# Kernel optimization log

Hardware: AMD Instinct MI355X
Metric: run time of the kernel (lower is better)

Reference implementation:

```python
import jax, jax.numpy as jnp
import numpy as np

SEQ, BATCH, D_MODEL = 1536, 2, 1024
N_HEAD, D_HEAD, N_ROLL = 16, 64, 3
SCALE = 1.0 / float(np.sqrt(D_HEAD))
EPS_DENOM = 1e-5
EPS_LN = 1e-5


def _dpfp(x, n_roll=N_ROLL):
    # relu feature map: cat(relu(x), relu(-x)), then roll-multiply expansion
    x = jnp.concatenate([jax.nn.relu(x), jax.nn.relu(-x)], axis=-1)  # [S,B,N,2D]
    return jnp.concatenate(
        [x * jnp.roll(x, shift=i, axis=-1) for i in range(1, n_roll + 1)], axis=-1
    )  # [S,B,N,2D*n_roll]


def setup_inputs() -> dict:
    key = jax.random.key(0)
    k_h, k_q, k_kv, k_o = jax.random.split(key, 4)
    std = 1.0 / float(np.sqrt(D_MODEL))
    h = jax.random.normal(k_h, (SEQ, BATCH, D_MODEL), jnp.float32)
    Wq = jax.random.normal(k_q, (N_HEAD * D_HEAD, D_MODEL), jnp.float32) * std
    Wkv = jax.random.normal(k_kv, (2 * N_HEAD * D_HEAD, D_MODEL), jnp.float32) * std
    Wo = jax.random.normal(k_o, (D_MODEL, N_HEAD * D_HEAD), jnp.float32) * std
    ln_gamma = jnp.ones((D_MODEL,), jnp.float32)
    ln_beta = jnp.zeros((D_MODEL,), jnp.float32)
    # Transformer-XL causal mask: triu(ones(qlen, klen), 1)[:, :, None] -> dim 3
    attn_mask = jnp.triu(jnp.ones((SEQ, SEQ), bool), k=1)[:, :, None]
    return {"h": h, "Wq": Wq, "Wkv": Wkv, "Wo": Wo,
            "ln_gamma": ln_gamma, "ln_beta": ln_beta, "attn_mask": attn_mask}


def reference(h, Wq, Wkv, Wo, ln_gamma, ln_beta, attn_mask):
    S, B, _ = h.shape
    # projections (no mems, post-lnorm, eval mode -> dropout identity)
    q = (h @ Wq.T).reshape(S, B, N_HEAD, D_HEAD)
    k, v = jnp.split(h @ Wkv.T, 2, axis=-1)
    k = k.reshape(S, B, N_HEAD, D_HEAD)
    v = v.reshape(S, B, N_HEAD, D_HEAD)
    # DPFP feature maps -> feature dim 2*D_HEAD*N_ROLL
    q = _dpfp(q)
    k = _dpfp(k)
    # kernelized scores [S,S,B,N]
    score = jnp.einsum('ibnd,jbnd->ijbn', q, k) * SCALE
    # 3-D mask [qlen,klen,1] -> broadcast over (b via size-1) and heads
    score = jnp.where(attn_mask[:, :, :, None], 0.0, score)
    # sum-normalization over keys (axis 1 = j)
    denom = jnp.sum(score, axis=1, keepdims=True) + EPS_DENOM
    prob = score / denom
    attn_vec = jnp.einsum('ijbn,jbnd->ibnd', prob, v).reshape(S, B, N_HEAD * D_HEAD)
    attn_out = attn_vec @ Wo.T
    # post-layernorm residual
    x = h + attn_out
    mean = jnp.mean(x, axis=-1, keepdims=True)
    var = jnp.var(x, axis=-1, keepdims=True)
    return ln_gamma * (x - mean) / jnp.sqrt(var + EPS_LN) + ln_beta
```

## Files before the change

### kernel.cpp

```cpp
#include <hip/hip_runtime.h>
#include <hip/hip_bf16.h>

#define S_LEN 1536
#define BATCH 2
#define DMODEL 1024
#define NHEAD 16
#define DHEAD 64
#define FDIM 384
#define CHUNK 64
#define NCHUNK 24
#define ROWS (S_LEN*BATCH)
#define SCALE_F 0.125f
#define EPS_D 1e-5f
#define EPS_LN 1e-5f

typedef unsigned short u16;
typedef __attribute__((ext_vector_type(8))) __bf16 bf16x8;
typedef __attribute__((ext_vector_type(8))) unsigned short ushort8;
typedef __attribute__((ext_vector_type(4))) float f32x4;

static __device__ __forceinline__ float bf2f(u16 a) {
  return __uint_as_float(((unsigned)a) << 16);
}
static __device__ __forceinline__ u16 f2bf(float x) {
  unsigned u = __float_as_uint(x);
  unsigned r = (u + 0x7FFFu + ((u >> 16) & 1u)) >> 16;
  return (u16)r;
}
static __device__ __forceinline__ void gload_lds16(const void* g, void* l) {
  __builtin_amdgcn_global_load_lds(
      (const __attribute__((address_space(1))) void*)g,
      (__attribute__((address_space(3))) void*)l, 16, 0, 0);
}
#define MFMA(a, b, c) __builtin_amdgcn_mfma_f32_16x16x32_bf16(a, b, c, 0, 0, 0)


__global__ __launch_bounds__(256) void cvt_all(
    const float* __restrict__ h, const float* __restrict__ Wq,
    const float* __restrict__ Wkv, const float* __restrict__ Wo,
    u16* __restrict__ h_bf, u16* __restrict__ Wqkv_bf, u16* __restrict__ Wo_bf) {
  int i = blockIdx.x * 256 + threadIdx.x;
  const float* src; u16* dst; int j;
  if (i < 786432) { src = h; dst = h_bf; j = i; }
  else if (i < 1048576) { src = Wq; dst = Wqkv_bf; j = i - 786432; }
  else if (i < 1572864) { src = Wkv; dst = Wqkv_bf + 1048576; j = i - 1048576; }
  else { src = Wo; dst = Wo_bf; j = i - 1572864; }
  float4 v = ((const float4*)src)[j];
  ushort4 o = {f2bf(v.x), f2bf(v.y), f2bf(v.z), f2bf(v.w)};
  ((ushort4*)dst)[j] = o;
}

__global__ __launch_bounds__(256) void gemm_bf16_mfma(
    const u16* __restrict__ A, const u16* __restrict__ B,
    float* __restrict__ C, int M, int N, int K) {
  __shared__ u16 As[128 * 32];
  __shared__ u16 Bs[128 * 32];
  const int t = threadIdx.x;
  const int l = t & 63, w = t >> 6;
  const int nbx = gridDim.x;
  const int fl = blockIdx.y * nbx + blockIdx.x;
  const int q8 = (nbx * gridDim.y) >> 3;
  const int fl2 = (fl & 7) * q8 + (fl >> 3);
  const int m0 = (fl2 / nbx) * 128, n0 = (fl2 % nbx) * 128;
  const int wm = (w >> 1) * 64, wn = (w & 1) * 64;

  f32x4 acc[4][4];
#pragma unroll
  for (int i = 0; i < 4; ++i)
#pragma unroll
    for (int j = 0; j < 4; ++j) acc[i][j] = (f32x4)0.f;

  const size_t Kb = (size_t)K * 2;
  const int o_lo = w * 1024 + l * 16;
  const int o_hi = 4096 + w * 1024 + l * 16;
  const int r_lo = o_lo >> 6, kb_lo = o_lo & 63;
  const int r_hi = o_hi >> 6, kb_hi = o_hi & 63;

  const char* Ap0 = (const char*)A + (size_t)(m0 + r_lo) * Kb + kb_lo;
  const char* Ap1 = (const char*)A + (size_t)(m0 + r_hi) * Kb + kb_hi;
  const char* Bp0 = (const char*)B + (size_t)(n0 + r_lo) * Kb + kb_lo;
  const char* Bp1 = (const char*)B + (size_t)(n0 + r_hi) * Kb + kb_hi;
  u16* AsB0 = As + (w * 1024) / 2;
  u16* AsB1 = As + (4096 + w * 1024) / 2;
  u16* BsB0 = Bs + (w * 1024) / 2;
  u16* BsB1 = Bs + (4096 + w * 1024) / 2;

  const int fr = l & 15, ko = (l >> 4) * 8;

  for (int k0 = 0; k0 < K; k0 += 32) {
    __syncthreads();
    gload_lds16(Ap0, AsB0);
    gload_lds16(Ap1, AsB1);
    gload_lds16(Bp0, BsB0);
    gload_lds16(Bp1, BsB1);
    Ap0 += 64; Ap1 += 64; Bp0 += 64; Bp1 += 64;
    __syncthreads();
    bf16x8 a[4], b[4];
#pragma unroll
    for (int m = 0; m < 4; ++m)
      a[m] = *(const bf16x8*)&As[(wm + m * 16 + fr) * 32 + ko];
#pragma unroll
    for (int n = 0; n < 4; ++n)
      b[n] = *(const bf16x8*)&Bs[(wn + n * 16 + fr) * 32 + ko];
#pragma unroll
    for (int m = 0; m < 4; ++m)
#pragma unroll
      for (int n = 0; n < 4; ++n)
        acc[m][n] = MFMA(a[m], b[n], acc[m][n]);
  }

  const int cr = (l >> 4) * 4, ccol = l & 15;
#pragma unroll
  for (int m = 0; m < 4; ++m)
#pragma unroll
    for (int n = 0; n < 4; ++n)
#pragma unroll
      for (int j = 0; j < 4; ++j)
        C[(size_t)(m0 + wm + m * 16 + cr + j) * N + (n0 + wn + n * 16 + ccol)] =
            acc[m][n][j];
}

__global__ __launch_bounds__(256) void gemm64_bf16(
    const u16* __restrict__ A, const u16* __restrict__ B,
    float* __restrict__ C, int M, int N, int K) {
  __shared__ u16 As[64 * 32];
  __shared__ u16 Bs[64 * 32];
  const int t = threadIdx.x;
  const int l = t & 63, w = t >> 6;
  const int nbx = gridDim.x;
  const int fl = blockIdx.y * nbx + blockIdx.x;
  const int q8 = (nbx * gridDim.y) >> 3;
  const int fl2 = (fl & 7) * q8 + (fl >> 3);
  const int m0 = (fl2 / nbx) * 64, n0 = (fl2 % nbx) * 64;
  const int fr = l & 15, kg = l >> 4;
  const size_t Kb = (size_t)K * 2;
  const int o = t * 16, r = o >> 6, kb = o & 63;
  const char* Ap = (const char*)A + (size_t)(m0 + r) * Kb + kb;
  const char* Bp = (const char*)B + (size_t)(n0 + r) * Kb + kb;
  u16* AsB = As + (w * 1024) / 2;
  u16* BsB = Bs + (w * 1024) / 2;
  f32x4 acc[4];
#pragma unroll
  for (int i = 0; i < 4; ++i) acc[i] = (f32x4)0.f;
  for (int k0 = 0; k0 < K; k0 += 32) {
    __syncthreads();
    gload_lds16(Ap, AsB);
    gload_lds16(Bp, BsB);
    Ap += 64; Bp += 64;
    __syncthreads();
    bf16x8 a = *(const bf16x8*)&As[(16 * w + fr) * 32 + kg * 8];
#pragma unroll
    for (int nt = 0; nt < 4; ++nt) {
      bf16x8 b = *(const bf16x8*)&Bs[(16 * nt + fr) * 32 + kg * 8];
      acc[nt] = MFMA(a, b, acc[nt]);
    }
  }
#pragma unroll
  for (int nt = 0; nt < 4; ++nt)
#pragma unroll
    for (int reg = 0; reg < 4; ++reg)
      C[(size_t)(m0 + 16 * w + 4 * kg + reg) * N + (n0 + 16 * nt + fr)] =
          acc[nt][reg];
}

__global__ __launch_bounds__(256) void dpfp_q64(
    const float* __restrict__ proj, u16* __restrict__ qft) {
  const int c = blockIdx.x, bn = blockIdx.y;
  const int b = bn >> 4, n = bn & 15;
  const int s0 = c * CHUNK;
  const int t = threadIdx.x;
  __shared__ float y[64][129];
  const int j = t >> 2, dq = (t & 3) << 4;
  const float* qp = proj + (size_t)((s0 + j) * BATCH + b) * 3072 + n * DHEAD + dq;
#pragma unroll
  for (int u = 0; u < 4; ++u) {
    float4 xv = *(const float4*)(qp + 4 * u);
    int d = dq + 4 * u;
    y[j][d + 0] = fmaxf(xv.x, 0.f); y[j][64 + d + 0] = fmaxf(-xv.x, 0.f);
    y[j][d + 1] = fmaxf(xv.y, 0.f); y[j][64 + d + 1] = fmaxf(-xv.y, 0.f);
    y[j][d + 2] = fmaxf(xv.z, 0.f); y[j][64 + d + 2] = fmaxf(-xv.z, 0.f);
    y[j][d + 3] = fmaxf(xv.w, 0.f); y[j][64 + d + 3] = fmaxf(-xv.w, 0.f);
  }
  __syncthreads();
  u16* base = qft + (size_t)bn * 589824;
  const int fr = t & 15, kg = (t >> 4) & 3, l = t & 63;
#pragma unroll 2
  for (int it = 0; it < 12; ++it) {
    int tile = it * 4 + (t >> 6);
    int rT = tile / 12, cB = tile % 12;
    int sl = rT * 16 + fr;
    ushort8 o;
#pragma unroll
    for (int e = 0; e < 8; ++e) {
      int f = cB * 32 + kg * 8 + e, m = f & 127, sh = (f >> 7) + 1;
      o[e] = f2bf(y[sl][m] * y[sl][(m - sh) & 127]);
    }
    *(ushort8*)(base + ((size_t)(4 * c + rT) * 12 + cB) * 512 + l * 8) = o;
  }
}

__global__ __launch_bounds__(256) void dpfp_k64(
    const float* __restrict__ proj, u16* __restrict__ kft,
    u16* __restrict__ kfTt, u16* __restrict__ vTt) {
  const int c = blockIdx.x, bn = blockIdx.y;
  const int b = bn >> 4, n = bn & 15;
  const int s0 = c * CHUNK;
  const int t = threadIdx.x;
  __shared__ float y[64][129];
  __shared__ float vs[64][65];
  const int j = t >> 2, dq = (t & 3) << 4;
  const float* kp = proj + (size_t)((s0 + j) * BATCH + b) * 3072 + n * DHEAD + dq;
#pragma unroll
  for (int u = 0; u < 4; ++u) {
    float4 xv = *(const float4*)(kp + 1024 + 4 * u);
    float4 vv = *(const float4*)(kp + 2048 + 4 * u);
    int d = dq + 4 * u;
    y[j][d + 0] = fmaxf(xv.x, 0.f); y[j][64 + d + 0] = fmaxf(-xv.x, 0.f);
    y[j][d + 1] = fmaxf(xv.y, 0.f); y[j][64 + d + 1] = fmaxf(-xv.y, 0.f);
    y[j][d + 2] = fmaxf(xv.z, 0.f); y[j][64 + d + 2] = fmaxf(-xv.z, 0.f);
    y[j][d + 3] = fmaxf(xv.w, 0.f); y[j][64 + d + 3] = fmaxf(-xv.w, 0.f);
    vs[j][d + 0] = vv.x; vs[j][d + 1] = vv.y;
    vs[j][d + 2] = vv.z; vs[j][d + 3] = vv.w;
  }
  __syncthreads();
  const int fr = t & 15, kg = (t >> 4) & 3, l = t & 63;
  {
    u16* base = kft + (size_t)bn * 589824;
#pragma unroll 2
    for (int it = 0; it < 12; ++it) {
      int tile = it * 4 + (t >> 6);
      int rT = tile / 12, cB = tile % 12;
      int sl = rT * 16 + fr;
      ushort8 o;
#pragma unroll
      for (int e = 0; e < 8; ++e) {
        int f = cB * 32 + kg * 8 + e, m = f & 127, sh = (f >> 7) + 1;
        o[e] = f2bf(y[sl][m] * y[sl][(m - sh) & 127]);
      }
      *(ushort8*)(base + ((size_t)(4 * c + rT) * 12 + cB) * 512 + l * 8) = o;
    }
  }
  {
    u16* base = kfTt + (size_t)bn * 589824;
#pragma unroll 2
    for (int it = 0; it < 12; ++it) {
      int tile = it * 4 + (t >> 6);
      int rT = tile >> 1, cHalf = tile & 1;
      int f = rT * 16 + fr, m = f & 127, sh = (f >> 7) + 1;
      int sb = cHalf * 32 + kg * 8;
      ushort8 o;
#pragma unroll
      for (int e = 0; e < 8; ++e)
        o[e] = f2bf(y[sb + e][m] * y[sb + e][(m - sh) & 127]);
      *(ushort8*)(base + ((size_t)rT * 48 + 2 * c + cHalf) * 512 + l * 8) = o;
    }
  }
  {
    u16* base = vTt + (size_t)bn * 98304;
#pragma unroll
    for (int it = 0; it < 2; ++it) {
      int tile = it * 4 + (t >> 6);
      int rT = tile >> 1, cHalf = tile & 1;
      int d = rT * 16 + fr;
      int sb = cHalf * 32 + kg * 8;
      ushort8 o;
#pragma unroll
      for (int e = 0; e < 8; ++e) o[e] = f2bf(vs[sb + e][d]);
      *(ushort8*)(base + ((size_t)rT * 48 + 2 * c + cHalf) * 512 + l * 8) = o;
    }
  }
}

__global__ __launch_bounds__(256) void chunk_kv_scan(
    const u16* __restrict__ kfTt, const u16* __restrict__ vTt,
    u16* __restrict__ kvswz, float* __restrict__ ksumst) {
  const int fl = blockIdx.x;
  const int fl2 = (fl & 7) * 48 + (fl >> 3);
  const int bn = fl2 / 12, ft2 = fl2 % 12;
  const int t = threadIdx.x, l = t & 63, w = t >> 6;
  const int fr = l & 15, kg = l >> 4;
  const u16* vt_base = vTt + (size_t)bn * 98304;
  const u16* kt_base = kfTt + (size_t)bn * 589824;

  __shared__ u16 Ys[64][40];

  f32x4 pacc0 = (f32x4)0.f, pacc1 = (f32x4)0.f;
  float pks = 0.f;

  for (int c = 0; c < NCHUNK; ++c) {
    f32x4 acc0 = (f32x4)0.f, acc1 = (f32x4)0.f;
    float ksp = 0.f;
#pragma unroll
    for (int ksi = 0; ksi < 2; ++ksi) {
      bf16x8 a = *(const bf16x8*)(vt_base + ((size_t)w * 48 + 2 * c + ksi) * 512 + l * 8);
      const u16* bp0 = kt_base + ((size_t)(2 * ft2 + 0) * 48 + 2 * c + ksi) * 512 + l * 8;
      const u16* bp1 = kt_base + ((size_t)(2 * ft2 + 1) * 48 + 2 * c + ksi) * 512 + l * 8;
      bf16x8 b0 = *(const bf16x8*)bp0;
      bf16x8 b1 = *(const bf16x8*)bp1;
      if (w == 0) {
        ushort8 raw = *(const ushort8*)bp0;
#pragma unroll
        for (int e = 0; e < 8; ++e) ksp += bf2f(raw[e]);
      } else if (w == 1) {
        ushort8 raw = *(const ushort8*)bp1;
#pragma unroll
        for (int e = 0; e < 8; ++e) ksp += bf2f(raw[e]);
      }
      acc0 = MFMA(a, b0, acc0);
      acc1 = MFMA(a, b1, acc1);
    }
    __syncthreads();
#pragma unroll
    for (int reg = 0; reg < 4; ++reg) {
      Ys[16 * w + 4 * kg + reg][fr] = f2bf(pacc0[reg]);
      Ys[16 * w + 4 * kg + reg][16 + fr] = f2bf(pacc1[reg]);
    }
    __syncthreads();
    {
      ushort8 o = *(const ushort8*)&Ys[w * 16 + fr][kg * 8];
      *(ushort8*)(kvswz + (size_t)(bn * NCHUNK + c) * 24576 +
                  (size_t)(w * 12 + ft2) * 512 + l * 8) = o;
    }
    if (w < 2) {
      float x = ksp;
      x += __shfl_xor(x, 16);
      x += __shfl_xor(x, 32);
      if (kg == 0)
        ksumst[(size_t)(bn * NCHUNK + c) * FDIM + ft2 * 32 + w * 16 + fr] = pks;
      pks += x;
    }
    pacc0 += acc0;
    pacc1 += acc1;
  }
}

__global__ __launch_bounds__(256) void attn_mfma(
    const u16* __restrict__ qft, const u16* __restrict__ kft,
    const u16* __restrict__ vTt, const u16* __restrict__ kvswz,
    const float* __restrict__ kspre, u16* __restrict__ attnvec) {
  const int c = blockIdx.x, bn = blockIdx.y;
  const int b = bn >> 4, n = bn & 15;
  const int s0 = c * CHUNK;
  const int t = threadIdx.x, l = t & 63, w = t >> 6;
  const int fr = l & 15, kg = l >> 4;

  const u16* qbase = qft + (size_t)bn * 589824;
  const u16* kbase = kft + (size_t)bn * 589824;
  const u16* vbase = vTt + (size_t)bn * 98304;
  const u16* kvbase = kvswz + (size_t)(bn * NCHUNK + c) * 24576;
  const float* ksp = kspre + (size_t)(bn * NCHUNK + c) * FDIM;

  __shared__ u16 Sb[64][70];

  f32x4 acc[9];
#pragma unroll
  for (int i = 0; i < 9; ++i) acc[i] = (f32x4)0.f;

#pragma unroll 3
  for (int cB = 0; cB < 12; ++cB) {
    bf16x8 a = *(const bf16x8*)(qbase + ((size_t)(4 * c + w) * 12 + cB) * 512 + l * 8);
#pragma unroll
    for (int nt = 0; nt < 4; ++nt) {
      bf16x8 bfrag = *(const bf16x8*)(kbase + ((size_t)(4 * c + nt) * 12 + cB) * 512 + l * 8);
      acc[nt] = MFMA(a, bfrag, acc[nt]);
    }
#pragma unroll
    for (int nt = 0; nt < 4; ++nt) {
      bf16x8 bfrag = *(const bf16x8*)(kvbase + ((size_t)nt * 12 + cB) * 512 + l * 8);
      acc[4 + nt] = MFMA(a, bfrag, acc[4 + nt]);
    }
    ushort8 bd = {0, 0, 0, 0, 0, 0, 0, 0};
    if (fr == 0) {
#pragma unroll
      for (int e = 0; e < 8; ++e) bd[e] = f2bf(ksp[cB * 32 + kg * 8 + e]);
    }
    union { ushort8 u; bf16x8 v; } cu;
    cu.u = bd;
    acc[8] = MFMA(a, cu.v, acc[8]);
  }

  float rsum[4];
#pragma unroll
  for (int reg = 0; reg < 4; ++reg) {
    int i = 16 * w + 4 * kg + reg;
    float r = 0.f;
#pragma unroll
    for (int nt = 0; nt < 4; ++nt) {
      int jj = 16 * nt + fr;
      float sval = (jj <= i) ? acc[nt][reg] : 0.f;
      acc[nt][reg] = sval;
      r += sval;
    }
    r += __shfl_xor(r, 1); r += __shfl_xor(r, 2);
    r += __shfl_xor(r, 4); r += __shfl_xor(r, 8);
    rsum[reg] = r;
  }
#pragma unroll
  for (int nt = 0; nt < 4; ++nt)
#pragma unroll
    for (int reg = 0; reg < 4; ++reg)
      Sb[16 * w + 4 * kg + reg][16 * nt + fr] = f2bf(acc[nt][reg]);

  __syncthreads();

#pragma unroll
  for (int ksi = 0; ksi < 2; ++ksi) {
    const int ko = ksi * 32 + kg * 8;
    bf16x8 a = *(const bf16x8*)&Sb[16 * w + fr][ko];
#pragma unroll
    for (int nt = 0; nt < 4; ++nt) {
      bf16x8 bfrag = *(const bf16x8*)(vbase + ((size_t)nt * 48 + 2 * c + ksi) * 512 + l * 8);
      acc[4 + nt] = MFMA(a, bfrag, acc[4 + nt]);
    }
  }

#pragma unroll
  for (int reg = 0; reg < 4; ++reg) {
    int i = 16 * w + 4 * kg + reg;
    float dinter = __shfl(acc[8][reg], l & 48);
    float den = rsum[reg] + dinter;
    float sc = SCALE_F / (SCALE_F * den + EPS_D);
    int rowg = (s0 + i) * BATCH + b;
    u16* orow = attnvec + (size_t)rowg * DMODEL + n * DHEAD;
#pragma unroll
    for (int nt = 0; nt < 4; ++nt)
      orow[16 * nt + fr] = f2bf(acc[4 + nt][reg] * sc);
  }
}

__global__ __launch_bounds__(256) void ln_kernel(
    const float* __restrict__ h, const float* __restrict__ ao,
    const float* __restrict__ gamma, const float* __restrict__ beta,
    float* __restrict__ out) {
  const int r = blockIdx.x, t = threadIdx.x;
  const float* hr = h + (size_t)r * DMODEL;
  const float* ar = ao + (size_t)r * DMODEL;
  float4 xh = *(const float4*)(hr + t * 4);
  float4 xa = *(const float4*)(ar + t * 4);
  float4 x = {xh.x + xa.x, xh.y + xa.y, xh.z + xa.z, xh.w + xa.w};
  float sum = x.x + x.y + x.z + x.w;
  float sq = x.x * x.x + x.y * x.y + x.z * x.z + x.w * x.w;
#pragma unroll
  for (int o = 32; o >= 1; o >>= 1) {
    sum += __shfl_xor(sum, o);
    sq += __shfl_xor(sq, o);
  }
  __shared__ float s_sum[4], s_sq[4];
  int w = t >> 6;
  if ((t & 63) == 0) { s_sum[w] = sum; s_sq[w] = sq; }
  __syncthreads();
  sum = s_sum[0] + s_sum[1] + s_sum[2] + s_sum[3];
  sq = s_sq[0] + s_sq[1] + s_sq[2] + s_sq[3];
  float mean = sum * (1.0f / DMODEL);
  float var = sq * (1.0f / DMODEL) - mean * mean;
  float rstd = rsqrtf(var + EPS_LN);
  float4 g = *(const float4*)(gamma + t * 4);
  float4 bb = *(const float4*)(beta + t * 4);
  float4 o4 = {g.x * (x.x - mean) * rstd + bb.x,
               g.y * (x.y - mean) * rstd + bb.y,
               g.z * (x.z - mean) * rstd + bb.z,
               g.w * (x.w - mean) * rstd + bb.w};
  *(float4*)(out + (size_t)r * DMODEL + t * 4) = o4;
}

extern "C" void kernel_launch(void* const* d_in, const int* in_sizes, int n_in,
                              void* d_out, int out_size, void* d_ws, size_t ws_size,
                              hipStream_t stream) {
  const float* h = (const float*)d_in[0];
  const float* Wq = (const float*)d_in[1];
  const float* Wkv = (const float*)d_in[2];
  const float* Wo = (const float*)d_in[3];
  const float* gamma = (const float*)d_in[4];
  const float* beta = (const float*)d_in[5];
  float* out = (float*)d_out;

  float* ws = (float*)d_ws;
  float* proj = ws;
  u16* qft = (u16*)(proj + 9437184);
  u16* kft = qft + 18874368;
  u16* kfTt = kft + 18874368;
  u16* vTt = kfTt + 18874368;
  u16* kvswz = vTt + 3145728;
  float* ksumst = (float*)(kvswz + 18874368);
  u16* Wo_bf = (u16*)(ksumst + 294912);
  u16* h_bf = kvswz;
  u16* Wqkv_bf = kvswz + 3145728;
  u16* attnvec = (u16*)proj;
  float* attnout = proj + 1572864;

  hipLaunchKernelGGL(cvt_all, dim3(7168), dim3(256), 0, stream,
                     h, Wq, Wkv, Wo, h_bf, Wqkv_bf, Wo_bf);
  hipLaunchKernelGGL(gemm_bf16_mfma, dim3(24, 24), dim3(256), 0, stream,
                     h_bf, Wqkv_bf, proj, ROWS, 3072, 1024);
  hipLaunchKernelGGL(dpfp_q64, dim3(24, 32), dim3(256), 0, stream, proj, qft);
  hipLaunchKernelGGL(dpfp_k64, dim3(24, 32), dim3(256), 0, stream,
                     proj, kft, kfTt, vTt);
  hipLaunchKernelGGL(chunk_kv_scan, dim3(384), dim3(256), 0, stream,
                     kfTt, vTt, kvswz, ksumst);
  hipLaunchKernelGGL(attn_mfma, dim3(24, 32), dim3(256), 0, stream,
                     qft, kft, vTt, kvswz, ksumst, attnvec);
  hipLaunchKernelGGL(gemm64_bf16, dim3(16, 48), dim3(256), 0, stream,
                     attnvec, Wo_bf, attnout, ROWS, 1024, 1024);
  hipLaunchKernelGGL(ln_kernel, dim3(3072), dim3(256), 0, stream,
                     h, attnout, gamma, beta, out);
}
```

Baseline: 152.2 us.

## Compute DPFP features on the fly in scan and attention kernels

Removes the materialised q/k DPFP feature buffers (qft, kft, kfTt). The chunk scan and attention kernels now rebuild the 384-wide roll-product features from the 128-wide relu values staged in LDS as bf16. This trades large global writes and reads of the feature tensors for extra ALU and LDS work per MFMA fragment. The K relu staging is recomputed once per chunk in the scan and once per block in attention. Relu values are rounded to bf16 before the product, which slightly changes numerics.

Result: slower. 226.4 us (+48.8%).

```diff
diff --git a/kernel.cpp b/kernel.cpp
--- a/kernel.cpp
+++ b/kernel.cpp
@@ -34,6 +34,44 @@
 }
 #define MFMA(a, b, c) __builtin_amdgcn_mfma_f32_16x16x32_bf16(a, b, c, 0, 0, 0)
 
+static __device__ __forceinline__ void unpk(unsigned u, float& lo, float& hi) {
+  lo = __uint_as_float(u << 16);
+  hi = __uint_as_float(u & 0xffff0000u);
+}
+
+static __device__ __forceinline__ bf16x8 feat_frag(
+    const u16* __restrict__ yrow, int m, int SH) {
+  union U { ushort8 v; unsigned u[4]; };
+  U y1, y0;
+  y1.v = *(const ushort8*)(yrow + m);
+  y0.v = *(const ushort8*)(yrow + ((m - 8) & 127));
+  unsigned seq0 = y0.u[0], seq1 = y0.u[1], seq2 = y0.u[2], seq3 = y0.u[3];
+  unsigned seq4 = y1.u[0], seq5 = y1.u[1], seq6 = y1.u[2], seq7 = y1.u[3];
+  unsigned y2u[4];
+  if (SH == 2) {
+    y2u[0] = seq3; y2u[1] = seq4; y2u[2] = seq5; y2u[3] = seq6;
+  } else if (SH == 1) {
+    y2u[0] = (seq3 >> 16) | (seq4 << 16);
+    y2u[1] = (seq4 >> 16) | (seq5 << 16);
+    y2u[2] = (seq5 >> 16) | (seq6 << 16);
+    y2u[3] = (seq6 >> 16) | (seq7 << 16);
+  } else {
+    y2u[0] = (seq2 >> 16) | (seq3 << 16);
+    y2u[1] = (seq3 >> 16) | (seq4 << 16);
+    y2u[2] = (seq4 >> 16) | (seq5 << 16);
+    y2u[3] = (seq5 >> 16) | (seq6 << 16);
+  }
+  bf16x8 out;
+#pragma unroll
+  for (int i = 0; i < 4; ++i) {
+    float a0, a1, b0, b1;
+    unpk(y1.u[i], a0, a1);
+    unpk(y2u[i], b0, b1);
+    out[2 * i] = (__bf16)(a0 * b0);
+    out[2 * i + 1] = (__bf16)(a1 * b1);
+  }
+  return out;
+}
 
 __global__ __launch_bounds__(256) void cvt_all(
     const float* __restrict__ h, const float* __restrict__ Wq,
@@ -163,152 +201,119 @@
           acc[nt][reg];
 }
 
-__global__ __launch_bounds__(256) void dpfp_q64(
-    const float* __restrict__ proj, u16* __restrict__ qft) {
+__global__ __launch_bounds__(256) void dpfp_v(
+    const float* __restrict__ proj, u16* __restrict__ vTt) {
   const int c = blockIdx.x, bn = blockIdx.y;
   const int b = bn >> 4, n = bn & 15;
-  const int s0 = c * CHUNK;
   const int t = threadIdx.x;
-  __shared__ float y[64][129];
-  const int j = t >> 2, dq = (t & 3) << 4;
-  const float* qp = proj + (size_t)((s0 + j) * BATCH + b) * 3072 + n * DHEAD + dq;
-#pragma unroll
-  for (int u = 0; u < 4; ++u) {
-    float4 xv = *(const float4*)(qp + 4 * u);
-    int d = dq + 4 * u;
-    y[j][d + 0] = fmaxf(xv.x, 0.f); y[j][64 + d + 0] = fmaxf(-xv.x, 0.f);
-    y[j][d + 1] = fmaxf(xv.y, 0.f); y[j][64 + d + 1] = fmaxf(-xv.y, 0.f);
-    y[j][d + 2] = fmaxf(xv.z, 0.f); y[j][64 + d + 2] = fmaxf(-xv.z, 0.f);
-    y[j][d + 3] = fmaxf(xv.w, 0.f); y[j][64 + d + 3] = fmaxf(-xv.w, 0.f);
-  }
-  __syncthreads();
-  u16* base = qft + (size_t)bn * 589824;
-  const int fr = t & 15, kg = (t >> 4) & 3, l = t & 63;
-#pragma unroll 2
-  for (int it = 0; it < 12; ++it) {
-    int tile = it * 4 + (t >> 6);
-    int rT = tile / 12, cB = tile % 12;
-    int sl = rT * 16 + fr;
-    ushort8 o;
-#pragma unroll
-    for (int e = 0; e < 8; ++e) {
-      int f = cB * 32 + kg * 8 + e, m = f & 127, sh = (f >> 7) + 1;
-      o[e] = f2bf(y[sl][m] * y[sl][(m - sh) & 127]);
-    }
-    *(ushort8*)(base + ((size_t)(4 * c + rT) * 12 + cB) * 512 + l * 8) = o;
-  }
-}
-
-__global__ __launch_bounds__(256) void dpfp_k64(
-    const float* __restrict__ proj, u16* __restrict__ kft,
-    u16* __restrict__ kfTt, u16* __restrict__ vTt) {
-  const int c = blockIdx.x, bn = blockIdx.y;
-  const int b = bn >> 4, n = bn & 15;
-  const int s0 = c * CHUNK;
-  const int t = threadIdx.x;
-  __shared__ float y[64][129];
   __shared__ float vs[64][65];
   const int j = t >> 2, dq = (t & 3) << 4;
-  const float* kp = proj + (size_t)((s0 + j) * BATCH + b) * 3072 + n * DHEAD + dq;
+  const float* vp = proj + (size_t)((c * CHUNK + j) * BATCH + b) * 3072 +
+                    2048 + n * DHEAD + dq;
 #pragma unroll
   for (int u = 0; u < 4; ++u) {
-    float4 xv = *(const float4*)(kp + 1024 + 4 * u);
-    float4 vv = *(const float4*)(kp + 2048 + 4 * u);
+    float4 vv = *(const float4*)(vp + 4 * u);
     int d = dq + 4 * u;
-    y[j][d + 0] = fmaxf(xv.x, 0.f); y[j][64 + d + 0] = fmaxf(-xv.x, 0.f);
-    y[j][d + 1] = fmaxf(xv.y, 0.f); y[j][64 + d + 1] = fmaxf(-xv.y, 0.f);
-    y[j][d + 2] = fmaxf(xv.z, 0.f); y[j][64 + d + 2] = fmaxf(-xv.z, 0.f);
-    y[j][d + 3] = fmaxf(xv.w, 0.f); y[j][64 + d + 3] = fmaxf(-xv.w, 0.f);
     vs[j][d + 0] = vv.x; vs[j][d + 1] = vv.y;
     vs[j][d + 2] = vv.z; vs[j][d + 3] = vv.w;
   }
   __syncthreads();
   const int fr = t & 15, kg = (t >> 4) & 3, l = t & 63;
-  {
-    u16* base = kft + (size_t)bn * 589824;
-#pragma unroll 2
-    for (int it = 0; it < 12; ++it) {
-      int tile = it * 4 + (t >> 6);
-      int rT = tile / 12, cB = tile % 12;
-      int sl = rT * 16 + fr;
-      ushort8 o;
-#pragma unroll
-      for (int e = 0; e < 8; ++e) {
-        int f = cB * 32 + kg * 8 + e, m = f & 127, sh = (f >> 7) + 1;
-        o[e] = f2bf(y[sl][m] * y[sl][(m - sh) & 127]);
-      }
-      *(ushort8*)(base + ((size_t)(4 * c + rT) * 12 + cB) * 512 + l * 8) = o;
-    }
-  }
-  {
-    u16* base = kfTt + (size_t)bn * 589824;
-#pragma unroll 2
-    for (int it = 0; it < 12; ++it) {
-      int tile = it * 4 + (t >> 6);
-      int rT = tile >> 1, cHalf = tile & 1;
-      int f = rT * 16 + fr, m = f & 127, sh = (f >> 7) + 1;
-      int sb = cHalf * 32 + kg * 8;
-      ushort8 o;
-#pragma unroll
-      for (int e = 0; e < 8; ++e)
-        o[e] = f2bf(y[sb + e][m] * y[sb + e][(m - sh) & 127]);
-      *(ushort8*)(base + ((size_t)rT * 48 + 2 * c + cHalf) * 512 + l * 8) = o;
-    }
-  }
-  {
-    u16* base = vTt + (size_t)bn * 98304;
-#pragma unroll
-    for (int it = 0; it < 2; ++it) {
-      int tile = it * 4 + (t >> 6);
-      int rT = tile >> 1, cHalf = tile & 1;
-      int d = rT * 16 + fr;
-      int sb = cHalf * 32 + kg * 8;
-      ushort8 o;
-#pragma unroll
-      for (int e = 0; e < 8; ++e) o[e] = f2bf(vs[sb + e][d]);
-      *(ushort8*)(base + ((size_t)rT * 48 + 2 * c + cHalf) * 512 + l * 8) = o;
-    }
+  u16* base = vTt + (size_t)bn * 98304;
+#pragma unroll
+  for (int it = 0; it < 2; ++it) {
+    int tile = it * 4 + (t >> 6);
+    int rT = tile >> 1, cHalf = tile & 1;
+    int d = rT * 16 + fr;
+    int sb = cHalf * 32 + kg * 8;
+    ushort8 o;
+#pragma unroll
+    for (int e = 0; e < 8; ++e) o[e] = f2bf(vs[sb + e][d]);
+    *(ushort8*)(base + ((size_t)rT * 48 + 2 * c + cHalf) * 512 + l * 8) = o;
   }
 }
 
 __global__ __launch_bounds__(256) void chunk_kv_scan(
-    const u16* __restrict__ kfTt, const u16* __restrict__ vTt,
+    const float* __restrict__ proj, const u16* __restrict__ vTt,
     u16* __restrict__ kvswz, float* __restrict__ ksumst) {
   const int fl = blockIdx.x;
   const int fl2 = (fl & 7) * 48 + (fl >> 3);
   const int bn = fl2 / 12, ft2 = fl2 % 12;
+  const int b = bn >> 4, n = bn & 15;
   const int t = threadIdx.x, l = t & 63, w = t >> 6;
   const int fr = l & 15, kg = l >> 4;
   const u16* vt_base = vTt + (size_t)bn * 98304;
-  const u16* kt_base = kfTt + (size_t)bn * 589824;
-
+
+  __shared__ u16 yT[128][72];
   __shared__ u16 Ys[64][40];
+
+  const int sh = ft2 / 4 + 1;
+  const int f0 = 32 * ft2 + fr;
+  const int f1 = 32 * ft2 + 16 + fr;
+  const int m0r = f0 & 127, m0s = (m0r - sh) & 127;
+  const int m1r = f1 & 127, m1s = (m1r - sh) & 127;
+
+  const int j = t >> 2, dq = (t & 3) << 4;
 
   f32x4 pacc0 = (f32x4)0.f, pacc1 = (f32x4)0.f;
   float pks = 0.f;
 
   for (int c = 0; c < NCHUNK; ++c) {
+    {
+      const float* kp = proj + (size_t)(((c * CHUNK + j) * BATCH + b)) * 3072 +
+                        1024 + n * DHEAD + dq;
+#pragma unroll
+      for (int u = 0; u < 4; ++u) {
+        float4 xv = *(const float4*)(kp + 4 * u);
+        int d = dq + 4 * u;
+        yT[d + 0][j] = f2bf(fmaxf(xv.x, 0.f));
+        yT[d + 1][j] = f2bf(fmaxf(xv.y, 0.f));
+        yT[d + 2][j] = f2bf(fmaxf(xv.z, 0.f));
+        yT[d + 3][j] = f2bf(fmaxf(xv.w, 0.f));
+        yT[64 + d + 0][j] = f2bf(fmaxf(-xv.x, 0.f));
+        yT[64 + d + 1][j] = f2bf(fmaxf(-xv.y, 0.f));
+        yT[64 + d + 2][j] = f2bf(fmaxf(-xv.z, 0.f));
+        yT[64 + d + 3][j] = f2bf(fmaxf(-xv.w, 0.f));
+      }
+    }
+    __syncthreads();
+
     f32x4 acc0 = (f32x4)0.f, acc1 = (f32x4)0.f;
     float ksp = 0.f;
 #pragma unroll
     for (int ksi = 0; ksi < 2; ++ksi) {
+      const int so = ksi * 32 + kg * 8;
       bf16x8 a = *(const bf16x8*)(vt_base + ((size_t)w * 48 + 2 * c + ksi) * 512 + l * 8);
-      const u16* bp0 = kt_base + ((size_t)(2 * ft2 + 0) * 48 + 2 * c + ksi) * 512 + l * 8;
-      const u16* bp1 = kt_base + ((size_t)(2 * ft2 + 1) * 48 + 2 * c + ksi) * 512 + l * 8;
-      bf16x8 b0 = *(const bf16x8*)bp0;
-      bf16x8 b1 = *(const bf16x8*)bp1;
-      if (w == 0) {
-        ushort8 raw = *(const ushort8*)bp0;
-#pragma unroll
-        for (int e = 0; e < 8; ++e) ksp += bf2f(raw[e]);
-      } else if (w == 1) {
-        ushort8 raw = *(const ushort8*)bp1;
-#pragma unroll
-        for (int e = 0; e < 8; ++e) ksp += bf2f(raw[e]);
+      union U { ushort8 v; unsigned u[4]; };
+      U r1, r2;
+      bf16x8 b0, b1;
+      float s0 = 0.f, s1 = 0.f;
+      r1.v = *(const ushort8*)&yT[m0r][so];
+      r2.v = *(const ushort8*)&yT[m0s][so];
+#pragma unroll
+      for (int i = 0; i < 4; ++i) {
+        float a0, a1, c0, c1;
+        unpk(r1.u[i], a0, a1); unpk(r2.u[i], c0, c1);
+        float p0 = a0 * c0, p1 = a1 * c1;
+        s0 += p0 + p1;
+        b0[2 * i] = (__bf16)p0; b0[2 * i + 1] = (__bf16)p1;
       }
+      r1.v = *(const ushort8*)&yT[m1r][so];
+      r2.v = *(const ushort8*)&yT[m1s][so];
+#pragma unroll
+      for (int i = 0; i < 4; ++i) {
+        float a0, a1, c0, c1;
+        unpk(r1.u[i], a0, a1); unpk(r2.u[i], c0, c1);
+        float p0 = a0 * c0, p1 = a1 * c1;
+        s1 += p0 + p1;
+        b1[2 * i] = (__bf16)p0; b1[2 * i + 1] = (__bf16)p1;
+      }
+      if (w == 0) ksp += s0;
+      else if (w == 1) ksp += s1;
       acc0 = MFMA(a, b0, acc0);
       acc1 = MFMA(a, b1, acc1);
     }
+
     __syncthreads();
 #pragma unroll
     for (int reg = 0; reg < 4; ++reg) {
@@ -331,52 +336,84 @@
     }
     pacc0 += acc0;
     pacc1 += acc1;
+    __syncthreads();
   }
 }
 
 __global__ __launch_bounds__(256) void attn_mfma(
-    const u16* __restrict__ qft, const u16* __restrict__ kft,
-    const u16* __restrict__ vTt, const u16* __restrict__ kvswz,
-    const float* __restrict__ kspre, u16* __restrict__ attnvec) {
+    const float* __restrict__ proj, const u16* __restrict__ vTt,
+    const u16* __restrict__ kvswz, const float* __restrict__ kspre,
+    u16* __restrict__ attnvec) {
   const int c = blockIdx.x, bn = blockIdx.y;
   const int b = bn >> 4, n = bn & 15;
   const int s0 = c * CHUNK;
   const int t = threadIdx.x, l = t & 63, w = t >> 6;
   const int fr = l & 15, kg = l >> 4;
 
-  const u16* qbase = qft + (size_t)bn * 589824;
-  const u16* kbase = kft + (size_t)bn * 589824;
   const u16* vbase = vTt + (size_t)bn * 98304;
   const u16* kvbase = kvswz + (size_t)(bn * NCHUNK + c) * 24576;
   const float* ksp = kspre + (size_t)(bn * NCHUNK + c) * FDIM;
 
+  __shared__ u16 y_q[64][136];
+  __shared__ u16 y_k[64][136];
   __shared__ u16 Sb[64][70];
 
+  {
+    const int j = t >> 2, dq = (t & 3) << 4;
+    const float* qp = proj + (size_t)((s0 + j) * BATCH + b) * 3072 + n * DHEAD;
+#pragma unroll
+    for (int u = 0; u < 4; ++u) {
+      float4 xq = *(const float4*)(qp + dq + 4 * u);
+      float4 xk = *(const float4*)(qp + 1024 + dq + 4 * u);
+      int d = dq + 4 * u;
+      ushort4 qp4 = {f2bf(fmaxf(xq.x, 0.f)), f2bf(fmaxf(xq.y, 0.f)),
+                     f2bf(fmaxf(xq.z, 0.f)), f2bf(fmaxf(xq.w, 0.f))};
+      ushort4 qn4 = {f2bf(fmaxf(-xq.x, 0.f)), f2bf(fmaxf(-xq.y, 0.f)),
+                     f2bf(fmaxf(-xq.z, 0.f)), f2bf(fmaxf(-xq.w, 0.f))};
+      ushort4 kp4 = {f2bf(fmaxf(xk.x, 0.f)), f2bf(fmaxf(xk.y, 0.f)),
+                     f2bf(fmaxf(xk.z, 0.f)), f2bf(fmaxf(xk.w, 0.f))};
+      ushort4 kn4 = {f2bf(fmaxf(-xk.x, 0.f)), f2bf(fmaxf(-xk.y, 0.f)),
+                     f2bf(fmaxf(-xk.z, 0.f)), f2bf(fmaxf(-xk.w, 0.f))};
+      *(ushort4*)&y_q[j][d] = qp4;
+      *(ushort4*)&y_q[j][64 + d] = qn4;
+      *(ushort4*)&y_k[j][d] = kp4;
+      *(ushort4*)&y_k[j][64 + d] = kn4;
+    }
+  }
+  __syncthreads();
+
   f32x4 acc[9];
 #pragma unroll
   for (int i = 0; i < 9; ++i) acc[i] = (f32x4)0.f;
 
-#pragma unroll 3
-  for (int cB = 0; cB < 12; ++cB) {
-    bf16x8 a = *(const bf16x8*)(qbase + ((size_t)(4 * c + w) * 12 + cB) * 512 + l * 8);
-#pragma unroll
-    for (int nt = 0; nt < 4; ++nt) {
-      bf16x8 bfrag = *(const bf16x8*)(kbase + ((size_t)(4 * c + nt) * 12 + cB) * 512 + l * 8);
-      acc[nt] = MFMA(a, bfrag, acc[nt]);
-    }
-#pragma unroll
-    for (int nt = 0; nt < 4; ++nt) {
-      bf16x8 bfrag = *(const bf16x8*)(kvbase + ((size_t)nt * 12 + cB) * 512 + l * 8);
-      acc[4 + nt] = MFMA(a, bfrag, acc[4 + nt]);
-    }
-    ushort8 bd = {0, 0, 0, 0, 0, 0, 0, 0};
-    if (fr == 0) {
-#pragma unroll
-      for (int e = 0; e < 8; ++e) bd[e] = f2bf(ksp[cB * 32 + kg * 8 + e]);
-    }
-    union { ushort8 u; bf16x8 v; } cu;
-    cu.u = bd;
-    acc[8] = MFMA(a, cu.v, acc[8]);
+  const u16* yqrow = &y_q[16 * w + fr][0];
+
+#pragma unroll
+  for (int shb = 0; shb < 3; ++shb) {
+#pragma unroll
+    for (int q4 = 0; q4 < 4; ++q4) {
+      const int cB = shb * 4 + q4;
+      const int m = q4 * 32 + kg * 8;
+      bf16x8 a = feat_frag(yqrow, m, shb + 1);
+#pragma unroll
+      for (int nt = 0; nt < 4; ++nt) {
+        bf16x8 bk = feat_frag(&y_k[16 * nt + fr][0], m, shb + 1);
+        acc[nt] = MFMA(a, bk, acc[nt]);
+      }
+#pragma unroll
+      for (int nt = 0; nt < 4; ++nt) {
+        bf16x8 bfrag = *(const bf16x8*)(kvbase + ((size_t)nt * 12 + cB) * 512 + l * 8);
+        acc[4 + nt] = MFMA(a, bfrag, acc[4 + nt]);
+      }
+      ushort8 bd = {0, 0, 0, 0, 0, 0, 0, 0};
+      if (fr == 0) {
+#pragma unroll
+        for (int e = 0; e < 8; ++e) bd[e] = f2bf(ksp[cB * 32 + kg * 8 + e]);
+      }
+      union { ushort8 u; bf16x8 v; } cu;
+      cu.u = bd;
+      acc[8] = MFMA(a, cu.v, acc[8]);
+    }
   }
 
   float rsum[4];
@@ -476,29 +513,24 @@
 
   float* ws = (float*)d_ws;
   float* proj = ws;
-  u16* qft = (u16*)(proj + 9437184);
-  u16* kft = qft + 18874368;
-  u16* kfTt = kft + 18874368;
-  u16* vTt = kfTt + 18874368;
+  u16* vTt = (u16*)(proj + 9437184);
   u16* kvswz = vTt + 3145728;
   float* ksumst = (float*)(kvswz + 18874368);
   u16* Wo_bf = (u16*)(ksumst + 294912);
-  u16* h_bf = kvswz;
-  u16* Wqkv_bf = kvswz + 3145728;
-  u16* attnvec = (u16*)proj;
-  float* attnout = proj + 1572864;
+  u16* h_bf = Wo_bf + 1048576;
+  u16* Wqkv_bf = h_bf + 3145728;
+  u16* attnvec = Wqkv_bf + 3145728;
+  float* attnout = (float*)(attnvec + 3145728);
 
   hipLaunchKernelGGL(cvt_all, dim3(7168), dim3(256), 0, stream,
                      h, Wq, Wkv, Wo, h_bf, Wqkv_bf, Wo_bf);
   hipLaunchKernelGGL(gemm_bf16_mfma, dim3(24, 24), dim3(256), 0, stream,
                      h_bf, Wqkv_bf, proj, ROWS, 3072, 1024);
-  hipLaunchKernelGGL(dpfp_q64, dim3(24, 32), dim3(256), 0, stream, proj, qft);
-  hipLaunchKernelGGL(dpfp_k64, dim3(24, 32), dim3(256), 0, stream,
-                     proj, kft, kfTt, vTt);
+  hipLaunchKernelGGL(dpfp_v, dim3(24, 32), dim3(256), 0, stream, proj, vTt);
   hipLaunchKernelGGL(chunk_kv_scan, dim3(384), dim3(256), 0, stream,
-                     kfTt, vTt, kvswz, ksumst);
+                     proj, vTt, kvswz, ksumst);
   hipLaunchKernelGGL(attn_mfma, dim3(24, 32), dim3(256), 0, stream,
-                     qft, kft, vTt, kvswz, ksumst, attnvec);
+                     proj, vTt, kvswz, ksumst, attnvec);
   hipLaunchKernelGGL(gemm64_bf16, dim3(16, 48), dim3(256), 0, stream,
                      attnvec, Wo_bf, attnout, ROWS, 1024, 1024);
   hipLaunchKernelGGL(ln_kernel, dim3(3072), dim3(256), 0, stream,
```

## Recompute transposed DPFP key features inside the KV scan instead of materializing

Applied to the files above, without the earlier changes.

Removes the transposed key-feature tensor written by dpfp_k64. chunk_kv_scan now loads the raw fp32 key projection per chunk, applies relu/negated-relu into a transposed bf16 LDS tile, and forms the roll-product features and key sums on the fly before the MFMAs. This drops a large global write and reread of the feature tensor. In exchange, each scan block redoes the relu and product work for every chunk and adds an extra barrier per iteration. The workspace layout is reshuffled so that buffers which used to alias kvswz/proj no longer overlap.

New measurement: 173.6 us. 1.14x slower.

```diff
diff --git a/kernel.cpp b/kernel.cpp
--- a/kernel.cpp
+++ b/kernel.cpp
@@ -33,6 +33,11 @@
       (__attribute__((address_space(3))) void*)l, 16, 0, 0);
 }
 #define MFMA(a, b, c) __builtin_amdgcn_mfma_f32_16x16x32_bf16(a, b, c, 0, 0, 0)
+
+static __device__ __forceinline__ void unpk(unsigned u, float& lo, float& hi) {
+  lo = __uint_as_float(u << 16);
+  hi = __uint_as_float(u & 0xffff0000u);
+}
 
 
 __global__ __launch_bounds__(256) void cvt_all(
@@ -201,7 +206,7 @@
 
 __global__ __launch_bounds__(256) void dpfp_k64(
     const float* __restrict__ proj, u16* __restrict__ kft,
-    u16* __restrict__ kfTt, u16* __restrict__ vTt) {
+    u16* __restrict__ vTt) {
   const int c = blockIdx.x, bn = blockIdx.y;
   const int b = bn >> 4, n = bn & 15;
   const int s0 = c * CHUNK;
@@ -241,21 +246,6 @@
     }
   }
   {
-    u16* base = kfTt + (size_t)bn * 589824;
-#pragma unroll 2
-    for (int it = 0; it < 12; ++it) {
-      int tile = it * 4 + (t >> 6);
-      int rT = tile >> 1, cHalf = tile & 1;
-      int f = rT * 16 + fr, m = f & 127, sh = (f >> 7) + 1;
-      int sb = cHalf * 32 + kg * 8;
-      ushort8 o;
-#pragma unroll
-      for (int e = 0; e < 8; ++e)
-        o[e] = f2bf(y[sb + e][m] * y[sb + e][(m - sh) & 127]);
-      *(ushort8*)(base + ((size_t)rT * 48 + 2 * c + cHalf) * 512 + l * 8) = o;
-    }
-  }
-  {
     u16* base = vTt + (size_t)bn * 98304;
 #pragma unroll
     for (int it = 0; it < 2; ++it) {
@@ -272,43 +262,86 @@
 }
 
 __global__ __launch_bounds__(256) void chunk_kv_scan(
-    const u16* __restrict__ kfTt, const u16* __restrict__ vTt,
+    const float* __restrict__ proj, const u16* __restrict__ vTt,
     u16* __restrict__ kvswz, float* __restrict__ ksumst) {
   const int fl = blockIdx.x;
   const int fl2 = (fl & 7) * 48 + (fl >> 3);
   const int bn = fl2 / 12, ft2 = fl2 % 12;
+  const int b = bn >> 4, n = bn & 15;
   const int t = threadIdx.x, l = t & 63, w = t >> 6;
   const int fr = l & 15, kg = l >> 4;
   const u16* vt_base = vTt + (size_t)bn * 98304;
-  const u16* kt_base = kfTt + (size_t)bn * 589824;
-
+
+  __shared__ u16 yT[128][72];
   __shared__ u16 Ys[64][40];
+
+  const int sh = ft2 / 4 + 1;
+  const int f0 = 32 * ft2 + fr;
+  const int f1 = 32 * ft2 + 16 + fr;
+  const int m0r = f0 & 127, m0s = (m0r - sh) & 127;
+  const int m1r = f1 & 127, m1s = (m1r - sh) & 127;
+
+  const int j = t >> 2, dq = (t & 3) << 4;
 
   f32x4 pacc0 = (f32x4)0.f, pacc1 = (f32x4)0.f;
   float pks = 0.f;
 
   for (int c = 0; c < NCHUNK; ++c) {
+    {
+      const float* kp = proj + (size_t)(((c * CHUNK + j) * BATCH + b)) * 3072 +
+                        1024 + n * DHEAD + dq;
+#pragma unroll
+      for (int u = 0; u < 4; ++u) {
+        float4 xv = *(const float4*)(kp + 4 * u);
+        int d = dq + 4 * u;
+        yT[d + 0][j] = f2bf(fmaxf(xv.x, 0.f));
+        yT[d + 1][j] = f2bf(fmaxf(xv.y, 0.f));
+        yT[d + 2][j] = f2bf(fmaxf(xv.z, 0.f));
+        yT[d + 3][j] = f2bf(fmaxf(xv.w, 0.f));
+        yT[64 + d + 0][j] = f2bf(fmaxf(-xv.x, 0.f));
+        yT[64 + d + 1][j] = f2bf(fmaxf(-xv.y, 0.f));
+        yT[64 + d + 2][j] = f2bf(fmaxf(-xv.z, 0.f));
+        yT[64 + d + 3][j] = f2bf(fmaxf(-xv.w, 0.f));
+      }
+    }
+    __syncthreads();
+
     f32x4 acc0 = (f32x4)0.f, acc1 = (f32x4)0.f;
     float ksp = 0.f;
 #pragma unroll
     for (int ksi = 0; ksi < 2; ++ksi) {
+      const int so = ksi * 32 + kg * 8;
       bf16x8 a = *(const bf16x8*)(vt_base + ((size_t)w * 48 + 2 * c + ksi) * 512 + l * 8);
-      const u16* bp0 = kt_base + ((size_t)(2 * ft2 + 0) * 48 + 2 * c + ksi) * 512 + l * 8;
-      const u16* bp1 = kt_base + ((size_t)(2 * ft2 + 1) * 48 + 2 * c + ksi) * 512 + l * 8;
-      bf16x8 b0 = *(const bf16x8*)bp0;
-      bf16x8 b1 = *(const bf16x8*)bp1;
-      if (w == 0) {
-        ushort8 raw = *(const ushort8*)bp0;
-#pragma unroll
-        for (int e = 0; e < 8; ++e) ksp += bf2f(raw[e]);
-      } else if (w == 1) {
-        ushort8 raw = *(const ushort8*)bp1;
-#pragma unroll
-        for (int e = 0; e < 8; ++e) ksp += bf2f(raw[e]);
+      union U { ushort8 v; unsigned u[4]; };
+      U r1, r2;
+      bf16x8 b0, b1;
+      float s0 = 0.f, s1 = 0.f;
+      r1.v = *(const ushort8*)&yT[m0r][so];
+      r2.v = *(const ushort8*)&yT[m0s][so];
+#pragma unroll
+      for (int i = 0; i < 4; ++i) {
+        float a0, a1, c0, c1;
+        unpk(r1.u[i], a0, a1); unpk(r2.u[i], c0, c1);
+        float p0 = a0 * c0, p1 = a1 * c1;
+        s0 += p0 + p1;
+        b0[2 * i] = (__bf16)p0; b0[2 * i + 1] = (__bf16)p1;
       }
+      r1.v = *(const ushort8*)&yT[m1r][so];
+      r2.v = *(const ushort8*)&yT[m1s][so];
+#pragma unroll
+      for (int i = 0; i < 4; ++i) {
+        float a0, a1, c0, c1;
+        unpk(r1.u[i], a0, a1); unpk(r2.u[i], c0, c1);
+        float p0 = a0 * c0, p1 = a1 * c1;
+        s1 += p0 + p1;
+        b1[2 * i] = (__bf16)p0; b1[2 * i + 1] = (__bf16)p1;
+      }
+      if (w == 0) ksp += s0;
+      else if (w == 1) ksp += s1;
       acc0 = MFMA(a, b0, acc0);
       acc1 = MFMA(a, b1, acc1);
     }
+
     __syncthreads();
 #pragma unroll
     for (int reg = 0; reg < 4; ++reg) {
@@ -331,6 +364,7 @@
     }
     pacc0 += acc0;
     pacc1 += acc1;
+    __syncthreads();
   }
 }
 
@@ -478,15 +512,14 @@
   float* proj = ws;
   u16* qft = (u16*)(proj + 9437184);
   u16* kft = qft + 18874368;
-  u16* kfTt = kft + 18874368;
-  u16* vTt = kfTt + 18874368;
+  u16* vTt = kft + 18874368;
   u16* kvswz = vTt + 3145728;
   float* ksumst = (float*)(kvswz + 18874368);
   u16* Wo_bf = (u16*)(ksumst + 294912);
-  u16* h_bf = kvswz;
-  u16* Wqkv_bf = kvswz + 3145728;
-  u16* attnvec = (u16*)proj;
-  float* attnout = proj + 1572864;
+  u16* h_bf = Wo_bf + 1048576;
+  u16* Wqkv_bf = h_bf + 3145728;
+  u16* attnvec = Wqkv_bf + 3145728;
+  float* attnout = (float*)(attnvec + 3145728);
 
   hipLaunchKernelGGL(cvt_all, dim3(7168), dim3(256), 0, stream,
                      h, Wq, Wkv, Wo, h_bf, Wqkv_bf, Wo_bf);
@@ -494,9 +527,9 @@
                      h_bf, Wqkv_bf, proj, ROWS, 3072, 1024);
   hipLaunchKernelGGL(dpfp_q64, dim3(24, 32), dim3(256), 0, stream, proj, qft);
   hipLaunchKernelGGL(dpfp_k64, dim3(24, 32), dim3(256), 0, stream,
-                     proj, kft, kfTt, vTt);
+                     proj, kft, vTt);
   hipLaunchKernelGGL(chunk_kv_scan, dim3(384), dim3(256), 0, stream,
-                     kfTt, vTt, kvswz, ksumst);
+                     proj, vTt, kvswz, ksumst);
   hipLaunchKernelGGL(attn_mfma, dim3(24, 32), dim3(256), 0, stream,
                      qft, kft, vTt, kvswz, ksumst, attnvec);
   hipLaunchKernelGGL(gemm64_bf16, dim3(16, 48), dim3(256), 0, stream,
```
